# Kernel tuning notes

Measured on AMD Instinct MI355X. Metric: run time of the kernel, lower is better.

Reference implementation:

```python
import jax, jax.numpy as jnp
import numpy as np

N = 100000          # nodes
E = 3200000         # edges (avg degree 32)
F_IN = 128          # num_features
HID = 128           # hidden_channels
C = 8               # num_classes
G = 64              # graphs in batch
EPS = 1e-5


def setup_inputs() -> dict:
    key = jax.random.key(0)
    ks = jax.random.split(key, 10)
    x = jax.random.normal(ks[0], (N, F_IN), dtype=jnp.float32)
    edge_index = jax.random.randint(ks[1], (2, E), 0, N, dtype=jnp.int64)
    batch = jnp.sort(jax.random.randint(ks[2], (N,), 0, G, dtype=jnp.int64))
    # parameters
    glorot1 = float(np.sqrt(6.0 / (F_IN + HID)))
    W1 = jax.random.uniform(ks[3], (F_IN, HID), minval=-glorot1, maxval=glorot1, dtype=jnp.float32)
    conv1_bias = jnp.zeros((HID,), jnp.float32)
    bn_weight = jnp.ones((F_IN,), jnp.float32)
    bn_bias = jnp.zeros((F_IN,), jnp.float32)
    ln_weight = jnp.ones((HID,), jnp.float32)
    ln_bias = jnp.zeros((HID,), jnp.float32)
    glorot2 = float(np.sqrt(6.0 / (HID + C)))
    lin_W = jax.random.uniform(ks[4], (C, HID), minval=-glorot2, maxval=glorot2, dtype=jnp.float32)
    lin_b = jnp.zeros((C,), jnp.float32)
    return {"x": x, "edge_index": edge_index, "batch": batch,
            "bn_weight": bn_weight, "bn_bias": bn_bias,
            "W1": W1, "conv1_bias": conv1_bias,
            "ln_weight": ln_weight, "ln_bias": ln_bias,
            "lin_W": lin_W, "lin_b": lin_b}


def reference(x, edge_index, batch, bn_weight, bn_bias, W1, conv1_bias,
              ln_weight, ln_bias, lin_W, lin_b):
    n = x.shape[0]
    # BatchNorm1d over nodes (training-mode batch statistics, biased var)
    mu = x.mean(axis=0)
    var = x.var(axis=0)
    x = (x - mu) * jax.lax.rsqrt(var + EPS) * bn_weight + bn_bias
    # GCNConv: linear transform, add self-loops, symmetric normalization, scatter-add
    h = x @ W1                                   # [N, HID]
    loops = jnp.arange(n, dtype=edge_index.dtype)
    row = jnp.concatenate([edge_index[0], loops])  # source nodes
    col = jnp.concatenate([edge_index[1], loops])  # target nodes
    deg = jax.ops.segment_sum(jnp.ones_like(col, dtype=h.dtype), col, num_segments=N)
    dinv = jax.lax.rsqrt(deg)                    # deg >= 1 due to self-loops
    norm = dinv[row] * dinv[col]                 # [E+N]
    msg = h[row] * norm[:, None]                 # gather + scale
    h = jax.ops.segment_sum(msg, col, num_segments=N) + conv1_bias
    h = jax.nn.relu(h)
    # PyG LayerNorm, mode='graph', batch=None: normalize over the whole tensor
    h = h - h.mean()
    h = h * jax.lax.rsqrt(h.var() + EPS)
    h = h * ln_weight + ln_bias
    # global mean pool per graph
    counts = jax.ops.segment_sum(jnp.ones((n,), h.dtype), batch, num_segments=G)
    sums = jax.ops.segment_sum(h, batch, num_segments=G)
    g = sums / jnp.maximum(counts, 1.0)[:, None]  # [G, HID]
    return g @ lin_W.T + lin_b                    # [G, C]
```

## Files before the change

### kernel.cpp

```cpp
#include <hip/hip_runtime.h>

#define NN 100000
#define NE 3200000
#define F 128
#define NG 64
#define NC 8
#define EPSF 1e-5f

#define NB_SCAN 391
#define AGG_BLOCKS 25000
#define LDSTRIDE 136
#define BN_BLOCKS 1024

#define NBK 256
#define BNODES 391
#define BCAP 14336
#define CHUNK 4096
#define P1_BLOCKS ((NE + CHUNK - 1) / CHUNK)

typedef __attribute__((ext_vector_type(8))) short bf16x8;
typedef __attribute__((ext_vector_type(4))) float f32x4;

__device__ __forceinline__ float bfu2f_lo(unsigned int q) {
    return __uint_as_float(q << 16);
}
__device__ __forceinline__ float bfu2f_hi(unsigned int q) {
    return __uint_as_float(q & 0xFFFF0000u);
}
__device__ __forceinline__ unsigned short f2bf(float f) {
    unsigned int u = __float_as_uint(f);
    u = u + 0x7FFFu + ((u >> 16) & 1u);
    return (unsigned short)(u >> 16);
}

__global__ void bn_partial_k(const float* __restrict__ x, float* __restrict__ part,
                             int n, int rpb) {
    int tid = threadIdx.x, col = tid & 127, half = tid >> 7;
    int r0 = blockIdx.x * rpb, r1 = min(n, r0 + rpb);
    float s = 0.f, ss = 0.f;
    for (int r = r0 + half; r < r1; r += 2) {
        float v = x[(size_t)r * F + col];
        s += v; ss += v * v;
    }
    __shared__ float sh[512];
    sh[tid] = s; sh[256 + tid] = ss;
    __syncthreads();
    if (half == 0) {
        part[blockIdx.x * 256 + col]       = sh[col] + sh[col + 128];
        part[blockIdx.x * 256 + 128 + col] = sh[256 + col] + sh[256 + col + 128];
    }
}

__global__ void bn_finalize_k(const float* __restrict__ part,
                              const float* __restrict__ bnw, const float* __restrict__ bnb,
                              float* __restrict__ scale, float* __restrict__ shift, int n) {
    int col = blockIdx.x, tid = threadIdx.x;
    float s = 0.f, ss = 0.f;
    #pragma unroll
    for (int i = 0; i < 4; ++i) {
        int b = tid + i * 256;
        s  += part[b * 256 + col];
        ss += part[b * 256 + 128 + col];
    }
    __shared__ float shs[256], shss[256];
    shs[tid] = s; shss[tid] = ss;
    __syncthreads();
    for (int o = 128; o > 0; o >>= 1) {
        if (tid < o) { shs[tid] += shs[tid + o]; shss[tid] += shss[tid + o]; }
        __syncthreads();
    }
    if (tid == 0) {
        float mu  = shs[0] / (float)n;
        float var = shss[0] / (float)n - mu * mu;
        float rstd = rsqrtf(var + EPSF);
        float sc = bnw[col] * rstd;
        scale[col] = sc;
        shift[col] = bnb[col] - mu * sc;
    }
}

__global__ void prep_wpT_k(const float* __restrict__ W1, const float* __restrict__ scale,
                           unsigned short* __restrict__ WpT) {
    int idx = blockIdx.x * 256 + threadIdx.x;
    if (idx < F * F) {
        int k = idx >> 7, j = idx & 127;
        WpT[j * F + k] = f2bf(scale[k] * W1[idx]);
    }
}
__global__ void prep_s_k(const float* __restrict__ W1, const float* __restrict__ shift,
                         float* __restrict__ S) {
    int j = blockIdx.x, k = threadIdx.x;
    __shared__ float sh[128];
    sh[k] = shift[k] * W1[k * F + j];
    __syncthreads();
    for (int o = 64; o > 0; o >>= 1) {
        if (k < o) sh[k] += sh[k + o];
        __syncthreads();
    }
    if (k == 0) S[j] = sh[0];
}

__global__ __launch_bounds__(256) void bucket_k(const int* __restrict__ ei,
                                                int* __restrict__ bcur,
                                                unsigned int* __restrict__ bbuf) {
    __shared__ int cntl[NBK];
    __shared__ int basel[NBK];
    __shared__ int gbase[NBK];
    __shared__ unsigned int ent[CHUNK];
    __shared__ unsigned char bid[CHUNK];
    int tid = threadIdx.x;
    int e0 = blockIdx.x * CHUNK;
    int ecnt = min(NE - e0, CHUNK);
    cntl[tid] = 0;
    __syncthreads();
    int myr[16], myc[16], myl[16];
    #pragma unroll
    for (int k = 0; k < 16; ++k) {
        int i = tid + k * 256;
        if (i < ecnt) {
            int r = ei[e0 + i];
            int c = ei[NE + e0 + i];
            myr[k] = r; myc[k] = c;
            myl[k] = atomicAdd(&cntl[(unsigned)c / BNODES], 1);
        } else { myr[k] = -1; myc[k] = 0; myl[k] = 0; }
    }
    __syncthreads();
    int myv = cntl[tid];
    basel[tid] = myv;
    __syncthreads();
    for (int o = 1; o < 256; o <<= 1) {
        int t = (tid >= o) ? basel[tid - o] : 0;
        __syncthreads();
        basel[tid] += t;
        __syncthreads();
    }
    basel[tid] -= myv;
    gbase[tid] = atomicAdd(&bcur[tid], myv);
    __syncthreads();
    #pragma unroll
    for (int k = 0; k < 16; ++k) {
        if (myr[k] >= 0) {
            int b = (unsigned)myc[k] / BNODES;
            int s = basel[b] + myl[k];
            ent[s] = ((unsigned)myr[k] << 9) | (unsigned)(myc[k] - b * BNODES);
            bid[s] = (unsigned char)b;
        }
    }
    __syncthreads();
    for (int s = tid; s < ecnt; s += 256) {
        unsigned int v = ent[s];
        int b = bid[s];
        int idx = s - basel[b] + gbase[b];
        if (idx < BCAP) bbuf[(size_t)b * BCAP + idx] = v;
    }
}

__global__ void hist_k(const unsigned int* __restrict__ bbuf, const int* __restrict__ bcur,
                       int* __restrict__ cnt, float* __restrict__ dinv) {
    int b = blockIdx.x, tid = threadIdx.x;
    __shared__ int h[BNODES];
    for (int i = tid; i < BNODES; i += 256) h[i] = 0;
    __syncthreads();
    int nbase = b * BNODES;
    int m = min(bcur[b], BCAP);
    for (int i = tid; i < m; i += 256)
        atomicAdd(&h[bbuf[(size_t)b * BCAP + i] & 511u], 1);
    __syncthreads();
    int lim = min(BNODES, NN - nbase);
    for (int i = tid; i < lim; i += 256) {
        int d = h[i];
        cnt[nbase + i] = d;
        dinv[nbase + i] = rsqrtf((float)d + 1.0f);
    }
}

__global__ void scan1_k(const int* __restrict__ cnt, int* __restrict__ bsum, int n) {
    int tid = threadIdx.x;
    int i = blockIdx.x * 256 + tid;
    int v = (i < n) ? cnt[i] : 0;
    __shared__ int sh[256];
    sh[tid] = v; __syncthreads();
    for (int o = 128; o > 0; o >>= 1) {
        if (tid < o) sh[tid] += sh[tid + o];
        __syncthreads();
    }
    if (tid == 0) bsum[blockIdx.x] = sh[0];
}

__global__ void scan2_k(const int* __restrict__ bsum, int* __restrict__ boff,
                        int nb, int* __restrict__ offs) {
    int tid = threadIdx.x;
    __shared__ int sh[512];
    sh[tid] = (tid < nb) ? bsum[tid] : 0;
    __syncthreads();
    for (int o = 1; o < 512; o <<= 1) {
        int t = (tid >= o) ? sh[tid - o] : 0;
        __syncthreads();
        sh[tid] += t;
        __syncthreads();
    }
    if (tid < nb) boff[tid] = (tid == 0) ? 0 : sh[tid - 1];
    if (tid == 0) offs[NN] = sh[nb - 1];
}

__global__ void scan3_k(const int* __restrict__ cnt, const int* __restrict__ boff,
                        int* __restrict__ offs, int n) {
    int tid = threadIdx.x;
    int i = blockIdx.x * 256 + tid;
    int v = (i < n) ? cnt[i] : 0;
    __shared__ int sh[256];
    sh[tid] = v; __syncthreads();
    for (int o = 1; o < 256; o <<= 1) {
        int t = (tid >= o) ? sh[tid - o] : 0;
        __syncthreads();
        sh[tid] += t;
        __syncthreads();
    }
    if (i < n) offs[i] = boff[blockIdx.x] + sh[tid] - v;
}

__global__ void scatter2_k(const unsigned int* __restrict__ bbuf, const int* __restrict__ bcur,
                           const int* __restrict__ offs, int* __restrict__ srow) {
    int b = blockIdx.x, tid = threadIdx.x;
    __shared__ int cur[BNODES];
    for (int i = tid; i < BNODES; i += 256) cur[i] = 0;
    __syncthreads();
    int nbase = b * BNODES;
    int m = min(bcur[b], BCAP);
    for (int i = tid; i < m; i += 256) {
        unsigned int v = bbuf[(size_t)b * BCAP + i];
        int dstl = (int)(v & 511u);
        int pos = offs[nbase + dstl] + atomicAdd(&cur[dstl], 1);
        srow[pos] = (int)(v >> 9);
    }
}

__global__ __launch_bounds__(256) void gemm_k(const float* __restrict__ x,
                                              const unsigned short* __restrict__ WpT,
                                              const float* __restrict__ S,
                                              const float* __restrict__ dinv,
                                              unsigned short* __restrict__ hbf, int n) {
    __shared__ unsigned short wt[128 * LDSTRIDE];
    __shared__ unsigned short xt[64 * LDSTRIDE];
    int tid = threadIdx.x;
    int row0 = blockIdx.x * 64;
    for (int i = tid; i < 2048; i += 256) {
        int r = i >> 4, c = (i & 15) * 8;
        uint4 v = *(const uint4*)&WpT[r * F + c];
        *(uint4*)&wt[r * LDSTRIDE + c] = v;
    }
    for (int i = tid; i < 2048; i += 256) {
        int r = i >> 5, c = (i & 31) * 4;
        float4 v = make_float4(0.f, 0.f, 0.f, 0.f);
        if (row0 + r < n) v = *(const float4*)&x[(size_t)(row0 + r) * F + c];
        unsigned int p0 = (unsigned int)f2bf(v.x) | ((unsigned int)f2bf(v.y) << 16);
        unsigned int p1 = (unsigned int)f2bf(v.z) | ((unsigned int)f2bf(v.w) << 16);
        *(uint2*)&xt[r * LDSTRIDE + c] = make_uint2(p0, p1);
    }
    __syncthreads();
    int wv = tid >> 6, lane = tid & 63;
    int lm = lane & 15, lk = lane >> 4;
    bf16x8 afrag[4];
    #pragma unroll
    for (int kk = 0; kk < 4; ++kk)
        afrag[kk] = *(bf16x8*)&xt[(wv * 16 + lm) * LDSTRIDE + kk * 32 + lk * 8];
    float dv[4];
    #pragma unroll
    for (int j = 0; j < 4; ++j) {
        int r = row0 + wv * 16 + lk * 4 + j;
        dv[j] = (r < n) ? dinv[r] : 1.0f;
    }
    #pragma unroll
    for (int nt = 0; nt < 8; ++nt) {
        float sv = S[nt * 16 + lm];
        f32x4 acc = {sv, sv, sv, sv};
        #pragma unroll
        for (int kk = 0; kk < 4; ++kk) {
            bf16x8 b = *(bf16x8*)&wt[(nt * 16 + lm) * LDSTRIDE + kk * 32 + lk * 8];
            acc = __builtin_amdgcn_mfma_f32_16x16x32_bf16(afrag[kk], b, acc, 0, 0, 0);
        }
        #pragma unroll
        for (int j = 0; j < 4; ++j) {
            int r = row0 + wv * 16 + lk * 4 + j;
            if (r < n) hbf[(size_t)r * F + nt * 16 + lm] = f2bf(acc[j] * dv[j]);
        }
    }
}

__device__ __forceinline__ void add8(float* acc, uint4 q) {
    acc[0] += bfu2f_lo(q.x); acc[1] += bfu2f_hi(q.x);
    acc[2] += bfu2f_lo(q.y); acc[3] += bfu2f_hi(q.y);
    acc[4] += bfu2f_lo(q.z); acc[5] += bfu2f_hi(q.z);
    acc[6] += bfu2f_lo(q.w); acc[7] += bfu2f_hi(q.w);
}

__global__ __launch_bounds__(256) void agg_k(const uint4* __restrict__ hb4,
                                             const int* __restrict__ srow,
                                             const int* __restrict__ offs,
                                             const float* __restrict__ dinv,
                                             const float* __restrict__ bias,
                                             uint4* __restrict__ h2p4,
                                             float* __restrict__ lnpart, int n) {
    int lane = threadIdx.x & 63, wv = threadIdx.x >> 6;
    int node = blockIdx.x * 4 + wv;
    int cg = lane & 15;
    int sub = lane >> 4;
    float s_part = 0.f, ss_part = 0.f;
    if (node < n) {
        int st = offs[node], en = offs[node + 1];
        float di = dinv[node];
        float acc[8] = {0.f, 0.f, 0.f, 0.f, 0.f, 0.f, 0.f, 0.f};
        uint4 qs = hb4[(size_t)node * 16 + cg];
        if (sub == 0) add8(acc, qs);
        const uint4 qz = make_uint4(0u, 0u, 0u, 0u);
        for (int base = st; base < en; base += 64) {
            int m = en - base; if (m > 64) m = 64;
            int sv = (lane < m) ? srow[base + lane] : 0;
            int nq = (m + 3) >> 2;
            int k = 0;
            for (; k + 2 <= nq; k += 2) {
                int i0 = 4 * k + sub, i1 = i0 + 4;
                int sr0 = __shfl(sv, i0), sr1 = __shfl(sv, i1);
                bool v0 = i0 < m, v1 = i1 < m;
                uint4 q0 = hb4[(size_t)(v0 ? sr0 : node) * 16 + cg];
                uint4 q1 = hb4[(size_t)(v1 ? sr1 : node) * 16 + cg];
                if (!v0) q0 = qz;
                if (!v1) q1 = qz;
                add8(acc, q0);
                add8(acc, q1);
            }
            for (; k < nq; ++k) {
                int i0 = 4 * k + sub;
                int sr0 = __shfl(sv, i0);
                bool v0 = i0 < m;
                uint4 q0 = hb4[(size_t)(v0 ? sr0 : node) * 16 + cg];
                if (!v0) q0 = qz;
                add8(acc, q0);
            }
        }
        #pragma unroll
        for (int j = 0; j < 8; ++j) acc[j] += __shfl_xor(acc[j], 16);
        #pragma unroll
        for (int j = 0; j < 8; ++j) acc[j] += __shfl_xor(acc[j], 32);
        float4 b0 = *(const float4*)&bias[cg * 8];
        float4 b1 = *(const float4*)&bias[cg * 8 + 4];
        float bv[8] = {b0.x, b0.y, b0.z, b0.w, b1.x, b1.y, b1.z, b1.w};
        float r[8];
        #pragma unroll
        for (int j = 0; j < 8; ++j) r[j] = fmaxf(fmaf(acc[j], di, bv[j]), 0.f);
        if (sub == 0) {
            uint4 p;
            p.x = (unsigned int)f2bf(r[0]) | ((unsigned int)f2bf(r[1]) << 16);
            p.y = (unsigned int)f2bf(r[2]) | ((unsigned int)f2bf(r[3]) << 16);
            p.z = (unsigned int)f2bf(r[4]) | ((unsigned int)f2bf(r[5]) << 16);
            p.w = (unsigned int)f2bf(r[6]) | ((unsigned int)f2bf(r[7]) << 16);
            h2p4[(size_t)node * 16 + cg] = p;
            #pragma unroll
            for (int j = 0; j < 8; ++j) {
                s_part += r[j];
                ss_part += r[j] * r[j];
            }
        }
    }
    __shared__ float sh[512];
    sh[threadIdx.x] = s_part; sh[256 + threadIdx.x] = ss_part;
    __syncthreads();
    for (int o = 128; o > 0; o >>= 1) {
        if (threadIdx.x < o) {
            sh[threadIdx.x] += sh[threadIdx.x + o];
            sh[256 + threadIdx.x] += sh[256 + threadIdx.x + o];
        }
        __syncthreads();
    }
    if (threadIdx.x == 0) {
        lnpart[blockIdx.x * 2]     = sh[0];
        lnpart[blockIdx.x * 2 + 1] = sh[256];
    }
}

__global__ void ln_reduce_k(const float* __restrict__ lnpart, int nb,
                            float* __restrict__ lnstats) {
    int tid = threadIdx.x;
    double s = 0.0, ss = 0.0;
    for (int i = tid; i < nb; i += 256) {
        s  += (double)lnpart[2 * i];
        ss += (double)lnpart[2 * i + 1];
    }
    __shared__ double sh[512];
    sh[tid] = s; sh[256 + tid] = ss;
    __syncthreads();
    for (int o = 128; o > 0; o >>= 1) {
        if (tid < o) { sh[tid] += sh[tid + o]; sh[256 + tid] += sh[256 + tid + o]; }
        __syncthreads();
    }
    if (tid == 0) {
        double cnt = (double)NN * (double)F;
        double mu = sh[0] / cnt;
        double var = sh[256] / cnt - mu * mu;
        lnstats[0] = (float)mu;
        lnstats[1] = (float)(1.0 / sqrt(var + (double)EPSF));
    }
}

__global__ void pool1_k(const unsigned int* __restrict__ h2p, const int* __restrict__ batch,
                        float* __restrict__ gsum, int n) {
    int tid = threadIdx.x, cp = tid & 63, half = tid >> 6;
    int n0 = blockIdx.x * 256, n1 = min(n, n0 + 256);
    int r = n0 + half;
    if (r >= n1) return;
    int gcur = batch[r];
    float a0 = 0.f, a1 = 0.f;
    for (; r < n1; r += 4) {
        int g = batch[r];
        unsigned int q = h2p[(size_t)r * 64 + cp];
        if (g != gcur) {
            atomicAdd(&gsum[gcur * F + cp * 2], a0);
            atomicAdd(&gsum[gcur * F + cp * 2 + 1], a1);
            a0 = a1 = 0.f; gcur = g;
        }
        a0 += bfu2f_lo(q);
        a1 += bfu2f_hi(q);
    }
    atomicAdd(&gsum[gcur * F + cp * 2], a0);
    atomicAdd(&gsum[gcur * F + cp * 2 + 1], a1);
}

__global__ void pool2_k(const float* __restrict__ gsum, const int* __restrict__ batch,
                        const float* __restrict__ lnstats,
                        const float* __restrict__ lnw, const float* __restrict__ lnb,
                        const float* __restrict__ linW, const float* __restrict__ linb,
                        float* __restrict__ out, int n) {
    int g = blockIdx.x, tid = threadIdx.x;
    __shared__ int bounds[2];
    if (tid < 2) {
        int target = g + tid;
        int lo = 0, hi = n;
        while (lo < hi) {
            int mid = (lo + hi) >> 1;
            if (batch[mid] < target) lo = mid + 1; else hi = mid;
        }
        bounds[tid] = lo;
    }
    __syncthreads();
    int cg = bounds[1] - bounds[0];
    __shared__ float vals[128];
    float v = 0.f;
    if (cg > 0) {
        float m = gsum[g * F + tid] / (float)cg;
        v = (m - lnstats[0]) * lnstats[1] * lnw[tid] + lnb[tid];
    }
    vals[tid] = v;
    __syncthreads();
    if (tid < NC) {
        float o = linb[tid];
        for (int k = 0; k < F; ++k) o = fmaf(vals[k], linW[tid * F + k], o);
        out[g * NC + tid] = o;
    }
}

extern "C" void kernel_launch(void* const* d_in, const int* in_sizes, int n_in,
                              void* d_out, int out_size, void* d_ws, size_t ws_size,
                              hipStream_t stream) {
    const float* x     = (const float*)d_in[0];
    const int*   ei    = (const int*)d_in[1];
    const int*   batch = (const int*)d_in[2];
    const float* bnw   = (const float*)d_in[3];
    const float* bnb   = (const float*)d_in[4];
    const float* W1    = (const float*)d_in[5];
    const float* cbias = (const float*)d_in[6];
    const float* lnw   = (const float*)d_in[7];
    const float* lnb   = (const float*)d_in[8];
    const float* linW  = (const float*)d_in[9];
    const float* linb  = (const float*)d_in[10];
    float* out = (float*)d_out;

    char* w = (char*)d_ws;
    size_t used = 0;
    auto alloc = [&](size_t bytes) {
        char* p = w;
        size_t pad = (bytes + 255) & ~(size_t)255;
        w += pad;
        used += pad;
        return p;
    };
    size_t bucket_bytes = (size_t)NBK * BCAP * 4;
    size_t hbf_bytes    = (size_t)NN * F * 2;
    char* regionA = (char*)alloc(bucket_bytes > hbf_bytes ? bucket_bytes : hbf_bytes);
    unsigned int*   bbuf = (unsigned int*)regionA;
    unsigned short* hbf  = (unsigned short*)regionA;

    unsigned int* h2p = (unsigned int*)alloc((size_t)NN * F * 2);
    int*   srow    = (int*)alloc((size_t)NE * 4);
    int*   cnt     = (int*)alloc((size_t)NN * 4);
    int*   offs    = (int*)alloc((size_t)(NN + 1) * 4);
    float* dinv    = (float*)alloc((size_t)NN * 4);
    int*   bcur    = (int*)alloc(NBK * 4);
    float* bnpart  = (float*)alloc((size_t)BN_BLOCKS * 256 * 4);
    float* scale   = (float*)alloc(512);
    float* shift   = (float*)alloc(512);
    unsigned short* WpT = (unsigned short*)alloc(128 * 128 * 2);
    float* Svec    = (float*)alloc(512);
    int*   bsum    = (int*)alloc(512 * 4);
    int*   boff    = (int*)alloc(512 * 4);
    float* lnpart  = (float*)alloc((size_t)AGG_BLOCKS * 2 * 4);
    float* lnstats = (float*)alloc(256);
    float* gsum    = (float*)alloc((size_t)NG * F * 4);

    if (used > ws_size) {
        hipMemsetAsync(d_out, 0, (size_t)out_size * 4, stream);
        return;
    }

    hipMemsetAsync(bcur, 0, NBK * 4, stream);
    hipMemsetAsync(gsum, 0, (size_t)NG * F * 4, stream);

    int rpb = (NN + BN_BLOCKS - 1) / BN_BLOCKS;
    bn_partial_k<<<BN_BLOCKS, 256, 0, stream>>>(x, bnpart, NN, rpb);
    bn_finalize_k<<<128, 256, 0, stream>>>(bnpart, bnw, bnb, scale, shift, NN);
    prep_wpT_k<<<64, 256, 0, stream>>>(W1, scale, WpT);
    prep_s_k<<<128, 128, 0, stream>>>(W1, shift, Svec);

    bucket_k<<<P1_BLOCKS, 256, 0, stream>>>(ei, bcur, bbuf);
    hist_k<<<NBK, 256, 0, stream>>>(bbuf, bcur, cnt, dinv);
    scan1_k<<<NB_SCAN, 256, 0, stream>>>(cnt, bsum, NN);
    scan2_k<<<1, 512, 0, stream>>>(bsum, boff, NB_SCAN, offs);
    scan3_k<<<NB_SCAN, 256, 0, stream>>>(cnt, boff, offs, NN);
    scatter2_k<<<NBK, 256, 0, stream>>>(bbuf, bcur, offs, srow);

    gemm_k<<<(NN + 63) / 64, 256, 0, stream>>>(x, WpT, Svec, dinv, hbf, NN);
    agg_k<<<AGG_BLOCKS, 256, 0, stream>>>((const uint4*)hbf, srow, offs, dinv,
                                          cbias, (uint4*)h2p, lnpart, NN);
    ln_reduce_k<<<1, 256, 0, stream>>>(lnpart, AGG_BLOCKS, lnstats);
    pool1_k<<<(NN + 255) / 256, 256, 0, stream>>>(h2p, batch, gsum, NN);
    pool2_k<<<NG, 128, 0, stream>>>(gsum, batch, lnstats, lnw, lnb, linW, linb, out, NN);
}
```

Measured before the change: 298.0 us.

## Switch intermediates to fp16 with packed-half accumulation and fuse degree scan into histogram

The GEMM output and the aggregated activations are now stored as fp16 instead of bf16. The gather-aggregate loop accumulates with packed half2 adds and shuffles instead of unpacking each value to fp32. Separately, the three-kernel prefix scan over node degrees is replaced by a per-bucket exclusive scan of bucket counts plus an in-block scan inside the histogram kernel, which removes two launches and the cnt array. Accumulating in fp16 risks precision loss and overflow for high-degree nodes, since sums of up to about 32+ terms are kept in half precision.

```diff
diff --git a/kernel.cpp b/kernel.cpp
--- a/kernel.cpp
+++ b/kernel.cpp
@@ -7,7 +7,6 @@
 #define NC 8
 #define EPSF 1e-5f
 
-#define NB_SCAN 391
 #define AGG_BLOCKS 25000
 #define LDSTRIDE 136
 #define BN_BLOCKS 1024
@@ -20,17 +19,21 @@
 
 typedef __attribute__((ext_vector_type(8))) short bf16x8;
 typedef __attribute__((ext_vector_type(4))) float f32x4;
-
-__device__ __forceinline__ float bfu2f_lo(unsigned int q) {
-    return __uint_as_float(q << 16);
-}
-__device__ __forceinline__ float bfu2f_hi(unsigned int q) {
-    return __uint_as_float(q & 0xFFFF0000u);
-}
+typedef _Float16 f16x2 __attribute__((ext_vector_type(2)));
+
+union U32H2 { unsigned int u; f16x2 h; };
+__device__ __forceinline__ f16x2 asH2(unsigned int u) { U32H2 c; c.u = u; return c.h; }
+__device__ __forceinline__ unsigned int asU32(f16x2 h) { U32H2 c; c.h = h; return c.u; }
+
 __device__ __forceinline__ unsigned short f2bf(float f) {
     unsigned int u = __float_as_uint(f);
     u = u + 0x7FFFu + ((u >> 16) & 1u);
     return (unsigned short)(u >> 16);
+}
+__device__ __forceinline__ unsigned short f2h_bits(float f) {
+    union { _Float16 h; unsigned short u; } c;
+    c.h = (_Float16)f;
+    return c.u;
 }
 
 __global__ void bn_partial_k(const float* __restrict__ x, float* __restrict__ part,
@@ -155,68 +158,52 @@
     }
 }
 
-__global__ void hist_k(const unsigned int* __restrict__ bbuf, const int* __restrict__ bcur,
-                       int* __restrict__ cnt, float* __restrict__ dinv) {
+__global__ void bbase_k(const int* __restrict__ bcur, int* __restrict__ bbase,
+                        int* __restrict__ offs) {
+    int tid = threadIdx.x;
+    __shared__ int s[256];
+    int v = bcur[tid];
+    s[tid] = v;
+    __syncthreads();
+    for (int o = 1; o < 256; o <<= 1) {
+        int t = (tid >= o) ? s[tid - o] : 0;
+        __syncthreads();
+        s[tid] += t;
+        __syncthreads();
+    }
+    bbase[tid] = s[tid] - v;
+    if (tid == 255) offs[NN] = s[255];
+}
+
+__global__ void hist2_k(const unsigned int* __restrict__ bbuf, const int* __restrict__ bcur,
+                        const int* __restrict__ bbase,
+                        int* __restrict__ offs, float* __restrict__ dinv) {
     int b = blockIdx.x, tid = threadIdx.x;
-    __shared__ int h[BNODES];
-    for (int i = tid; i < BNODES; i += 256) h[i] = 0;
-    __syncthreads();
-    int nbase = b * BNODES;
+    __shared__ int h0[512], hA[512], hB[512];
+    h0[tid] = 0; h0[tid + 256] = 0;
+    __syncthreads();
     int m = min(bcur[b], BCAP);
     for (int i = tid; i < m; i += 256)
-        atomicAdd(&h[bbuf[(size_t)b * BCAP + i] & 511u], 1);
-    __syncthreads();
+        atomicAdd(&h0[bbuf[(size_t)b * BCAP + i] & 511u], 1);
+    __syncthreads();
+    hA[tid] = h0[tid]; hA[tid + 256] = h0[tid + 256];
+    __syncthreads();
+    int* src = hA; int* dst = hB;
+    for (int o = 1; o < 512; o <<= 1) {
+        int i0 = tid, i1 = tid + 256;
+        dst[i0] = src[i0] + ((i0 >= o) ? src[i0 - o] : 0);
+        dst[i1] = src[i1] + ((i1 >= o) ? src[i1 - o] : 0);
+        __syncthreads();
+        int* tmp = src; src = dst; dst = tmp;
+    }
+    int nbase = b * BNODES;
+    int base = bbase[b];
     int lim = min(BNODES, NN - nbase);
     for (int i = tid; i < lim; i += 256) {
-        int d = h[i];
-        cnt[nbase + i] = d;
+        int d = h0[i];
+        offs[nbase + i] = base + src[i] - d;
         dinv[nbase + i] = rsqrtf((float)d + 1.0f);
     }
-}
-
-__global__ void scan1_k(const int* __restrict__ cnt, int* __restrict__ bsum, int n) {
-    int tid = threadIdx.x;
-    int i = blockIdx.x * 256 + tid;
-    int v = (i < n) ? cnt[i] : 0;
-    __shared__ int sh[256];
-    sh[tid] = v; __syncthreads();
-    for (int o = 128; o > 0; o >>= 1) {
-        if (tid < o) sh[tid] += sh[tid + o];
-        __syncthreads();
-    }
-    if (tid == 0) bsum[blockIdx.x] = sh[0];
-}
-
-__global__ void scan2_k(const int* __restrict__ bsum, int* __restrict__ boff,
-                        int nb, int* __restrict__ offs) {
-    int tid = threadIdx.x;
-    __shared__ int sh[512];
-    sh[tid] = (tid < nb) ? bsum[tid] : 0;
-    __syncthreads();
-    for (int o = 1; o < 512; o <<= 1) {
-        int t = (tid >= o) ? sh[tid - o] : 0;
-        __syncthreads();
-        sh[tid] += t;
-        __syncthreads();
-    }
-    if (tid < nb) boff[tid] = (tid == 0) ? 0 : sh[tid - 1];
-    if (tid == 0) offs[NN] = sh[nb - 1];
-}
-
-__global__ void scan3_k(const int* __restrict__ cnt, const int* __restrict__ boff,
-                        int* __restrict__ offs, int n) {
-    int tid = threadIdx.x;
-    int i = blockIdx.x * 256 + tid;
-    int v = (i < n) ? cnt[i] : 0;
-    __shared__ int sh[256];
-    sh[tid] = v; __syncthreads();
-    for (int o = 1; o < 256; o <<= 1) {
-        int t = (tid >= o) ? sh[tid - o] : 0;
-        __syncthreads();
-        sh[tid] += t;
-        __syncthreads();
-    }
-    if (i < n) offs[i] = boff[blockIdx.x] + sh[tid] - v;
 }
 
 __global__ void scatter2_k(const unsigned int* __restrict__ bbuf, const int* __restrict__ bcur,
@@ -239,7 +226,7 @@
                                               const unsigned short* __restrict__ WpT,
                                               const float* __restrict__ S,
                                               const float* __restrict__ dinv,
-                                              unsigned short* __restrict__ hbf, int n) {
+                                              unsigned short* __restrict__ hf, int n) {
     __shared__ unsigned short wt[128 * LDSTRIDE];
     __shared__ unsigned short xt[64 * LDSTRIDE];
     int tid = threadIdx.x;
@@ -282,16 +269,9 @@
         #pragma unroll
         for (int j = 0; j < 4; ++j) {
             int r = row0 + wv * 16 + lk * 4 + j;
-            if (r < n) hbf[(size_t)r * F + nt * 16 + lm] = f2bf(acc[j] * dv[j]);
-        }
-    }
-}
-
-__device__ __forceinline__ void add8(float* acc, uint4 q) {
-    acc[0] += bfu2f_lo(q.x); acc[1] += bfu2f_hi(q.x);
-    acc[2] += bfu2f_lo(q.y); acc[3] += bfu2f_hi(q.y);
-    acc[4] += bfu2f_lo(q.z); acc[5] += bfu2f_hi(q.z);
-    acc[6] += bfu2f_lo(q.w); acc[7] += bfu2f_hi(q.w);
+            if (r < n) hf[(size_t)r * F + nt * 16 + lm] = f2h_bits(acc[j] * dv[j]);
+        }
+    }
 }
 
 __global__ __launch_bounds__(256) void agg_k(const uint4* __restrict__ hb4,
@@ -309,9 +289,11 @@
     if (node < n) {
         int st = offs[node], en = offs[node + 1];
         float di = dinv[node];
-        float acc[8] = {0.f, 0.f, 0.f, 0.f, 0.f, 0.f, 0.f, 0.f};
-        uint4 qs = hb4[(size_t)node * 16 + cg];
-        if (sub == 0) add8(acc, qs);
+        f16x2 a0 = {0.f16, 0.f16}, a1 = a0, a2 = a0, a3 = a0;
+        if (sub == 0) {
+            uint4 qs = hb4[(size_t)node * 16 + cg];
+            a0 += asH2(qs.x); a1 += asH2(qs.y); a2 += asH2(qs.z); a3 += asH2(qs.w);
+        }
         const uint4 qz = make_uint4(0u, 0u, 0u, 0u);
         for (int base = st; base < en; base += 64) {
             int m = en - base; if (m > 64) m = 64;
@@ -326,8 +308,8 @@
                 uint4 q1 = hb4[(size_t)(v1 ? sr1 : node) * 16 + cg];
                 if (!v0) q0 = qz;
                 if (!v1) q1 = qz;
-                add8(acc, q0);
-                add8(acc, q1);
+                a0 += asH2(q0.x); a1 += asH2(q0.y); a2 += asH2(q0.z); a3 += asH2(q0.w);
+                a0 += asH2(q1.x); a1 += asH2(q1.y); a2 += asH2(q1.z); a3 += asH2(q1.w);
             }
             for (; k < nq; ++k) {
                 int i0 = 4 * k + sub;
@@ -335,13 +317,19 @@
                 bool v0 = i0 < m;
                 uint4 q0 = hb4[(size_t)(v0 ? sr0 : node) * 16 + cg];
                 if (!v0) q0 = qz;
-                add8(acc, q0);
+                a0 += asH2(q0.x); a1 += asH2(q0.y); a2 += asH2(q0.z); a3 += asH2(q0.w);
             }
         }
-        #pragma unroll
-        for (int j = 0; j < 8; ++j) acc[j] += __shfl_xor(acc[j], 16);
-        #pragma unroll
-        for (int j = 0; j < 8; ++j) acc[j] += __shfl_xor(acc[j], 32);
+        a0 += asH2((unsigned int)__shfl_xor((int)asU32(a0), 16));
+        a1 += asH2((unsigned int)__shfl_xor((int)asU32(a1), 16));
+        a2 += asH2((unsigned int)__shfl_xor((int)asU32(a2), 16));
+        a3 += asH2((unsigned int)__shfl_xor((int)asU32(a3), 16));
+        a0 += asH2((unsigned int)__shfl_xor((int)asU32(a0), 32));
+        a1 += asH2((unsigned int)__shfl_xor((int)asU32(a1), 32));
+        a2 += asH2((unsigned int)__shfl_xor((int)asU32(a2), 32));
+        a3 += asH2((unsigned int)__shfl_xor((int)asU32(a3), 32));
+        float acc[8] = {(float)a0[0], (float)a0[1], (float)a1[0], (float)a1[1],
+                        (float)a2[0], (float)a2[1], (float)a3[0], (float)a3[1]};
         float4 b0 = *(const float4*)&bias[cg * 8];
         float4 b1 = *(const float4*)&bias[cg * 8 + 4];
         float bv[8] = {b0.x, b0.y, b0.z, b0.w, b1.x, b1.y, b1.z, b1.w};
@@ -350,10 +338,10 @@
         for (int j = 0; j < 8; ++j) r[j] = fmaxf(fmaf(acc[j], di, bv[j]), 0.f);
         if (sub == 0) {
             uint4 p;
-            p.x = (unsigned int)f2bf(r[0]) | ((unsigned int)f2bf(r[1]) << 16);
-            p.y = (unsigned int)f2bf(r[2]) | ((unsigned int)f2bf(r[3]) << 16);
-            p.z = (unsigned int)f2bf(r[4]) | ((unsigned int)f2bf(r[5]) << 16);
-            p.w = (unsigned int)f2bf(r[6]) | ((unsigned int)f2bf(r[7]) << 16);
+            p.x = asU32(f16x2{(_Float16)r[0], (_Float16)r[1]});
+            p.y = asU32(f16x2{(_Float16)r[2], (_Float16)r[3]});
+            p.z = asU32(f16x2{(_Float16)r[4], (_Float16)r[5]});
+            p.w = asU32(f16x2{(_Float16)r[6], (_Float16)r[7]});
             h2p4[(size_t)node * 16 + cg] = p;
             #pragma unroll
             for (int j = 0; j < 8; ++j) {
@@ -412,14 +400,14 @@
     float a0 = 0.f, a1 = 0.f;
     for (; r < n1; r += 4) {
         int g = batch[r];
-        unsigned int q = h2p[(size_t)r * 64 + cp];
+        f16x2 hp = asH2(h2p[(size_t)r * 64 + cp]);
         if (g != gcur) {
             atomicAdd(&gsum[gcur * F + cp * 2], a0);
             atomicAdd(&gsum[gcur * F + cp * 2 + 1], a1);
             a0 = a1 = 0.f; gcur = g;
         }
-        a0 += bfu2f_lo(q);
-        a1 += bfu2f_hi(q);
+        a0 += (float)hp[0];
+        a1 += (float)hp[1];
     }
     atomicAdd(&gsum[gcur * F + cp * 2], a0);
     atomicAdd(&gsum[gcur * F + cp * 2 + 1], a1);
@@ -484,24 +472,22 @@
         return p;
     };
     size_t bucket_bytes = (size_t)NBK * BCAP * 4;
-    size_t hbf_bytes    = (size_t)NN * F * 2;
-    char* regionA = (char*)alloc(bucket_bytes > hbf_bytes ? bucket_bytes : hbf_bytes);
+    size_t hf_bytes     = (size_t)NN * F * 2;
+    char* regionA = (char*)alloc(bucket_bytes > hf_bytes ? bucket_bytes : hf_bytes);
     unsigned int*   bbuf = (unsigned int*)regionA;
-    unsigned short* hbf  = (unsigned short*)regionA;
+    unsigned short* hf   = (unsigned short*)regionA;
 
     unsigned int* h2p = (unsigned int*)alloc((size_t)NN * F * 2);
     int*   srow    = (int*)alloc((size_t)NE * 4);
-    int*   cnt     = (int*)alloc((size_t)NN * 4);
     int*   offs    = (int*)alloc((size_t)(NN + 1) * 4);
     float* dinv    = (float*)alloc((size_t)NN * 4);
     int*   bcur    = (int*)alloc(NBK * 4);
+    int*   bbase   = (int*)alloc(NBK * 4);
     float* bnpart  = (float*)alloc((size_t)BN_BLOCKS * 256 * 4);
     float* scale   = (float*)alloc(512);
     float* shift   = (float*)alloc(512);
     unsigned short* WpT = (unsigned short*)alloc(128 * 128 * 2);
     float* Svec    = (float*)alloc(512);
-    int*   bsum    = (int*)alloc(512 * 4);
-    int*   boff    = (int*)alloc(512 * 4);
     float* lnpart  = (float*)alloc((size_t)AGG_BLOCKS * 2 * 4);
     float* lnstats = (float*)alloc(256);
     float* gsum    = (float*)alloc((size_t)NG * F * 4);
@@ -521,14 +507,12 @@
     prep_s_k<<<128, 128, 0, stream>>>(W1, shift, Svec);
 
     bucket_k<<<P1_BLOCKS, 256, 0, stream>>>(ei, bcur, bbuf);
-    hist_k<<<NBK, 256, 0, stream>>>(bbuf, bcur, cnt, dinv);
-    scan1_k<<<NB_SCAN, 256, 0, stream>>>(cnt, bsum, NN);
-    scan2_k<<<1, 512, 0, stream>>>(bsum, boff, NB_SCAN, offs);
-    scan3_k<<<NB_SCAN, 256, 0, stream>>>(cnt, boff, offs, NN);
+    bbase_k<<<1, 256, 0, stream>>>(bcur, bbase, offs);
+    hist2_k<<<NBK, 256, 0, stream>>>(bbuf, bcur, bbase, offs, dinv);
     scatter2_k<<<NBK, 256, 0, stream>>>(bbuf, bcur, offs, srow);
 
-    gemm_k<<<(NN + 63) / 64, 256, 0, stream>>>(x, WpT, Svec, dinv, hbf, NN);
-    agg_k<<<AGG_BLOCKS, 256, 0, stream>>>((const uint4*)hbf, srow, offs, dinv,
+    gemm_k<<<(NN + 63) / 64, 256, 0, stream>>>(x, WpT, Svec, dinv, hf, NN);
+    agg_k<<<AGG_BLOCKS, 256, 0, stream>>>((const uint4*)hf, srow, offs, dinv,
                                           cbias, (uint4*)h2p, lnpart, NN);
     ln_reduce_k<<<1, 256, 0, stream>>>(lnpart, AGG_BLOCKS, lnstats);
     pool1_k<<<(NN + 255) / 256, 256, 0, stream>>>(h2p, batch, gsum, NN);
```

Result: no change. 293.8 us (-1.4%).
